# Performance work log

Measured on AMD Instinct MI355X. Metric: run time of the kernel, lower is better.

## Reference

```python
import jax, jax.numpy as jnp
import numpy as np

IN_C, OUT_C, K, STRIDE, PAD = 128, 256, 3, 1, 1

def setup_inputs() -> dict:
    key = jax.random.key(0)
    kx, kw = jax.random.split(key)
    x = jax.random.normal(kx, (32, IN_C, 56, 56), dtype=jnp.float32)
    # xavier_uniform_ on W: bound = sqrt(6 / (fan_in + fan_out)), fan = C*K*K
    fan_in = IN_C * K * K
    fan_out = OUT_C * K * K
    bound = float(np.sqrt(6.0 / (fan_in + fan_out)))
    W = jax.random.uniform(kw, (OUT_C, IN_C, K, K), dtype=jnp.float32, minval=-bound, maxval=bound)
    b = jnp.zeros((OUT_C,), dtype=jnp.float32)
    return {"x": x, "W": W, "b": b}

def reference(x, W, b):
    # Direct conv: NCHW input, OIHW weights -> NCHW output
    out = jax.lax.conv_general_dilated(
        x, W,
        window_strides=(STRIDE, STRIDE),
        padding=[(PAD, PAD), (PAD, PAD)],
        dimension_numbers=("NCHW", "OIHW", "NCHW"),
    )
    return out + b[None, :, None, None]
```

## Files before the change

### kernel.cpp

```cpp
#include <hip/hip_runtime.h>


typedef unsigned short u16;
typedef _Float16 f16x8 __attribute__((ext_vector_type(8)));
typedef float f32x4 __attribute__((ext_vector_type(4)));

#define CIN    128
#define COUT   256
#define HW     56
#define NPIX   3136
#define TOTPIX 100352
#define NKT    18

#define WAITVM0 asm volatile("s_waitcnt vmcnt(0)" ::: "memory")
#define BARRIER asm volatile("s_barrier" ::: "memory")

__device__ __forceinline__ void gload16(const void* g, void* l) {
  __builtin_amdgcn_global_load_lds(
      (const __attribute__((address_space(1))) void*)g,
      (__attribute__((address_space(3))) void*)l, 16, 0, 0);
}

__device__ __forceinline__ u16 f2h(float f) {
  _Float16 h = (_Float16)f;
  return __builtin_bit_cast(u16, h);
}

__global__ void prep_w(const float* __restrict__ W, u16* __restrict__ Wt,
                       u16* __restrict__ zp) {
  int e = blockIdx.x * 256 + threadIdx.x;
  if (blockIdx.x == 0 && threadIdx.x < 128) zp[threadIdx.x] = 0;
  int j   = e & 7;
  int ocl = (e >> 3) & 127;
  int k8  = (e >> 10) & 7;
  int o   = (e >> 13) & 1;
  int t   = e >> 14;
  int oc = o * 128 + ocl;
  int ic = (t & 1) * 64 + k8 * 8 + j;
  Wt[e] = f2h(W[(oc * CIN + ic) * 9 + (t >> 1)]);
}

__global__ void prep_x(const float* __restrict__ x, u16* __restrict__ xt) {
  __shared__ unsigned int tile[64 * 65];
  int b = blockIdx.x;
  int n = b / 49;
  int hw0 = (b % 49) * 64;
  int tid = threadIdx.x;
  const float* xb = x + (size_t)n * CIN * NPIX + hw0;
  #pragma unroll
  for (int i = 0; i < 16; ++i) {
    int e = tid + i * 256;
    int icp = e >> 6;
    int pix = e & 63;
    float a = xb[(size_t)(2 * icp) * NPIX + pix];
    float c = xb[(size_t)(2 * icp + 1) * NPIX + pix];
    tile[pix * 65 + icp] = (unsigned)f2h(a) | ((unsigned)f2h(c) << 16);
  }
  __syncthreads();
  #pragma unroll
  for (int i = 0; i < 4; ++i) {
    int e = tid + i * 256;
    int g = e >> 6;
    int pix = e & 63;
    uint4 v;
    v.x = tile[pix * 65 + g * 4 + 0];
    v.y = tile[pix * 65 + g * 4 + 1];
    v.z = tile[pix * 65 + g * 4 + 2];
    v.w = tile[pix * 65 + g * 4 + 3];
    *(uint4*)(xt + ((size_t)(n * 16 + g) * NPIX + hw0 + pix) * 8) = v;
  }
}

__global__ __launch_bounds__(512, 4) void conv_mfma(
    const u16* __restrict__ Wt, const u16* __restrict__ xt,
    const float* __restrict__ bias, float* __restrict__ out,
    const u16* __restrict__ zp) {
  __shared__ __align__(16) u16 lds[24576];

  int tid  = threadIdx.x;
  int lane = tid & 63;
  int wv   = tid >> 6;
  int bid  = blockIdx.x;
  int wgid = (bid & 7) * 98 + (bid >> 3);
  int octile = wgid & 1;
  int ptile  = wgid >> 1;

  int wm = wv >> 2, wn = wv & 3;
  int l15 = lane & 15, lg = lane >> 4;

  int spix = tid & 255;
  int sk8  = tid >> 8;
  int p = ptile * 256 + spix;
  int n = p / NPIX, r = p % NPIX, y = r / HW, xx = r % HW;
  const char* xtb = (const char*)xt;
  const char* wsrc = (const char*)Wt + (size_t)octile * 16384 + tid * 16;
  const char* zpc = (const char*)zp;

  auto stageA = [&](int t) {
    const char* src = wsrc + (size_t)t * 32768;
    gload16(src, &lds[tid * 8]);
    gload16(src + 8192, &lds[tid * 8 + 4096]);
  };
  auto stageB = [&](int t) {
    int tap = t >> 1, ich = t & 1;
    int t3 = tap / 3;
    int dh = t3 - 1, dw = (tap - t3 * 3) - 1;
    int iy = y + dh, ix = xx + dw;
    bool ok = (unsigned)iy < HW && (unsigned)ix < HW;
    const char* s0 = ok
        ? xtb + ((size_t)(n * 16 + ich * 8 + sk8) * NPIX + (r + dh * HW + dw)) * 16
        : zpc;
    size_t step = ok ? (size_t)2 * NPIX * 16 : 0;
    #pragma unroll
    for (int i = 0; i < 4; ++i)
      gload16(s0 + i * step, &lds[8192 + ((sk8 + 2 * i) * 256 + spix) * 8]);
  };

  f32x4 acc[4][4] = {};

  auto compute = [&]() {
    #pragma unroll
    for (int kk = 0; kk < 2; ++kk) {
      const u16* ab = &lds[((kk * 4 + lg) * 128 + wm * 64 + l15) * 8];
      const u16* bb = &lds[8192 + ((kk * 4 + lg) * 256 + wn * 64 + l15) * 8];
      f16x8 af[4], bf[4];
      #pragma unroll
      for (int q = 0; q < 4; ++q) af[q] = *(const f16x8*)&ab[q * 128];
      #pragma unroll
      for (int q = 0; q < 4; ++q) bf[q] = *(const f16x8*)&bb[q * 128];
      __builtin_amdgcn_s_setprio(1);
      #pragma unroll
      for (int mq = 0; mq < 4; ++mq)
        #pragma unroll
        for (int nf = 0; nf < 4; ++nf)
          acc[mq][nf] = __builtin_amdgcn_mfma_f32_16x16x32_f16(
              af[mq], bf[nf], acc[mq][nf], 0, 0, 0);
      __builtin_amdgcn_s_setprio(0);
    }
  };

  stageA(0); stageB(0);
  WAITVM0; BARRIER;
  for (int t = 0; t < NKT; ++t) {
    compute();
    if (t + 1 < NKT) {
      BARRIER;
      stageA(t + 1); stageB(t + 1);
      WAITVM0; BARRIER;
    }
  }

  float* ob[4];
  #pragma unroll
  for (int nf = 0; nf < 4; ++nf) {
    int pp = ptile * 256 + wn * 64 + nf * 16 + l15;
    int nn = pp / NPIX, hw = pp % NPIX;
    ob[nf] = out + (size_t)nn * COUT * NPIX + hw;
  }
  #pragma unroll
  for (int mq = 0; mq < 4; ++mq) {
    int oc = octile * 128 + wm * 64 + mq * 16 + lg * 4;
    f32x4 bv = *(const f32x4*)&bias[oc];
    #pragma unroll
    for (int rr = 0; rr < 4; ++rr) {
      size_t row = (size_t)(oc + rr) * NPIX;
      #pragma unroll
      for (int nf = 0; nf < 4; ++nf)
        ob[nf][row] = acc[mq][nf][rr] + bv[rr];
    }
  }
}

__global__ void conv_naive(const float* __restrict__ x, const float* __restrict__ W,
                           const float* __restrict__ b, float* __restrict__ out) {
  int idx = blockIdx.x * 256 + threadIdx.x;
  int hw = idx % NPIX;
  int tmp = idx / NPIX;
  int oc = tmp % COUT;
  int n = tmp / COUT;
  int h = hw / HW, w = hw % HW;
  float acc = b[oc];
  for (int ic = 0; ic < CIN; ++ic) {
    const float* xr = x + (size_t)(n * CIN + ic) * NPIX;
    const float* wr = W + (size_t)(oc * CIN + ic) * 9;
    #pragma unroll
    for (int kh = 0; kh < 3; ++kh) {
      int ih = h + kh - 1;
      if ((unsigned)ih >= HW) continue;
      #pragma unroll
      for (int kw = 0; kw < 3; ++kw) {
        int iw = w + kw - 1;
        if ((unsigned)iw >= HW) continue;
        acc += xr[ih * HW + iw] * wr[kh * 3 + kw];
      }
    }
  }
  out[idx] = acc;
}

extern "C" void kernel_launch(void* const* d_in, const int* in_sizes, int n_in,
                              void* d_out, int out_size, void* d_ws, size_t ws_size,
                              hipStream_t stream) {
  const float* x = (const float*)d_in[0];
  const float* W = (const float*)d_in[1];
  const float* b = (const float*)d_in[2];
  float* out = (float*)d_out;

  const size_t ZP_OFF = 0;
  const size_t WT_OFF = 256;
  const size_t XT_OFF = 256 + 589824;
  const size_t NEED = XT_OFF + (size_t)TOTPIX * CIN * 2;

  if (ws_size < NEED) {
    conv_naive<<<TOTPIX * COUT / 256, 256, 0, stream>>>(x, W, b, out);
    return;
  }
  char* ws = (char*)d_ws;
  u16* zp = (u16*)(ws + ZP_OFF);
  u16* Wt = (u16*)(ws + WT_OFF);
  u16* xt = (u16*)(ws + XT_OFF);

  prep_w<<<1152, 256, 0, stream>>>(W, Wt, zp);
  prep_x<<<1568, 256, 0, stream>>>(x, xt);
  conv_mfma<<<784, 512, 0, stream>>>(Wt, xt, b, out, zp);
}
```

Measured before the change: 91.91 us.

## Load activation fragments directly from global and double-buffer weight tiles in LDS

Activation (B) operands are no longer staged through LDS. Each lane loads its f16x8 fragments directly from global memory, using precomputed base offsets and a bitmask of which taps are in bounds, with padding taps reading a shared zero buffer. Weight tiles are now double-buffered in LDS, so the next tile's load is issued before the current compute and the barrier before staging is dropped. This shrinks LDS use and removes a barrier per step, but global loads now sit directly in front of the MFMAs and neighbouring waves re-read overlapping activation data through cache instead of from shared LDS.

Result: slower. 104.6 us (+13.8%).

```diff
diff --git a/kernel.cpp b/kernel.cpp
--- a/kernel.cpp
+++ b/kernel.cpp
@@ -75,7 +75,7 @@
     const u16* __restrict__ Wt, const u16* __restrict__ xt,
     const float* __restrict__ bias, float* __restrict__ out,
     const u16* __restrict__ zp) {
-  __shared__ __align__(16) u16 lds[24576];
+  __shared__ __align__(16) u16 lds[16384];
 
   int tid  = threadIdx.x;
   int lane = tid & 63;
@@ -88,46 +88,58 @@
   int wm = wv >> 2, wn = wv & 3;
   int l15 = lane & 15, lg = lane >> 4;
 
-  int spix = tid & 255;
-  int sk8  = tid >> 8;
-  int p = ptile * 256 + spix;
-  int n = p / NPIX, r = p % NPIX, y = r / HW, xx = r % HW;
-  const char* xtb = (const char*)xt;
+  const char* xtb  = (const char*)xt;
+  const char* zpc  = (const char*)zp;
   const char* wsrc = (const char*)Wt + (size_t)octile * 16384 + tid * 16;
-  const char* zpc = (const char*)zp;
+
+  unsigned boff[4];
+  unsigned long long vmask = 0ull;
+  #pragma unroll
+  for (int nf = 0; nf < 4; ++nf) {
+    int p = ptile * 256 + wn * 64 + nf * 16 + l15;
+    int n = p / NPIX, r = p % NPIX, y = r / HW, x = r % HW;
+    boff[nf] = (unsigned)(((n * 16 + lg) * NPIX + r) * 16);
+    #pragma unroll
+    for (int tap = 0; tap < 9; ++tap) {
+      int dh = tap / 3 - 1, dw = tap % 3 - 1;
+      unsigned long long ok =
+          ((unsigned)(y + dh) < HW && (unsigned)(x + dw) < HW) ? 1ull : 0ull;
+      vmask |= ok << (nf * 9 + tap);
+    }
+  }
 
   auto stageA = [&](int t) {
     const char* src = wsrc + (size_t)t * 32768;
-    gload16(src, &lds[tid * 8]);
-    gload16(src + 8192, &lds[tid * 8 + 4096]);
+    u16* dst = &lds[(t & 1) * 8192 + tid * 8];
+    gload16(src, dst);
+    gload16(src + 8192, dst + 4096);
   };
-  auto stageB = [&](int t) {
+
+  f32x4 acc[4][4] = {};
+
+  stageA(0);
+  WAITVM0; BARRIER;
+
+  for (int t = 0; t < NKT; ++t) {
     int tap = t >> 1, ich = t & 1;
-    int t3 = tap / 3;
-    int dh = t3 - 1, dw = (tap - t3 * 3) - 1;
-    int iy = y + dh, ix = xx + dw;
-    bool ok = (unsigned)iy < HW && (unsigned)ix < HW;
-    const char* s0 = ok
-        ? xtb + ((size_t)(n * 16 + ich * 8 + sk8) * NPIX + (r + dh * HW + dw)) * 16
-        : zpc;
-    size_t step = ok ? (size_t)2 * NPIX * 16 : 0;
-    #pragma unroll
-    for (int i = 0; i < 4; ++i)
-      gload16(s0 + i * step, &lds[8192 + ((sk8 + 2 * i) * 256 + spix) * 8]);
-  };
-
-  f32x4 acc[4][4] = {};
-
-  auto compute = [&]() {
+    int dh = tap / 3 - 1, dw = tap % 3 - 1;
+    int sh16 = ((dh * HW + dw) + ich * 8 * NPIX) * 16;
+    const u16* abase = &lds[(t & 1) * 8192];
+    if (t + 1 < NKT) stageA(t + 1);
     #pragma unroll
     for (int kk = 0; kk < 2; ++kk) {
-      const u16* ab = &lds[((kk * 4 + lg) * 128 + wm * 64 + l15) * 8];
-      const u16* bb = &lds[8192 + ((kk * 4 + lg) * 256 + wn * 64 + l15) * 8];
-      f16x8 af[4], bf[4];
-      #pragma unroll
-      for (int q = 0; q < 4; ++q) af[q] = *(const f16x8*)&ab[q * 128];
-      #pragma unroll
-      for (int q = 0; q < 4; ++q) bf[q] = *(const f16x8*)&bb[q * 128];
+      f16x8 bf[4], af[4];
+      #pragma unroll
+      for (int nf = 0; nf < 4; ++nf) {
+        bool ok = (vmask >> (nf * 9 + tap)) & 1ull;
+        const char* sp = ok ? xtb + ((int)boff[nf] + sh16 + kk * 4 * NPIX * 16)
+                            : zpc;
+        bf[nf] = *(const f16x8*)sp;
+      }
+      #pragma unroll
+      for (int q = 0; q < 4; ++q)
+        af[q] = *(const f16x8*)
+            &abase[((kk * 4 + lg) * 128 + wm * 64 + q * 16 + l15) * 8];
       __builtin_amdgcn_s_setprio(1);
       #pragma unroll
       for (int mq = 0; mq < 4; ++mq)
@@ -137,17 +149,8 @@
               af[mq], bf[nf], acc[mq][nf], 0, 0, 0);
       __builtin_amdgcn_s_setprio(0);
     }
-  };
-
-  stageA(0); stageB(0);
-  WAITVM0; BARRIER;
-  for (int t = 0; t < NKT; ++t) {
-    compute();
-    if (t + 1 < NKT) {
-      BARRIER;
-      stageA(t + 1); stageB(t + 1);
-      WAITVM0; BARRIER;
-    }
+    WAITVM0;
+    BARRIER;
   }
 
   float* ob[4];
```

## Double-buffer LDS stages and switch to 32x32x16 MFMA with halved K-steps

Applied to the files above, without the earlier changes.

Splits each K tile into two half-depth stages, which doubles the stage count. These stages are double-buffered in LDS so the global-to-LDS loads for the next stage are issued before computing on the current one. This removes one barrier per step and overlaps memory with MFMA. The 16x16x32 MFMAs are replaced with 32x32x16 MFMAs (2x2 per wave), which cuts LDS fragment reads per FLOP. The cost is more loop iterations and barriers, and a changed output register mapping in the epilogue.

Measured after the change: 101.3 us. +10.3%, slower.

```diff
diff --git a/kernel.cpp b/kernel.cpp
--- a/kernel.cpp
+++ b/kernel.cpp
@@ -4,13 +4,14 @@
 typedef unsigned short u16;
 typedef _Float16 f16x8 __attribute__((ext_vector_type(8)));
 typedef float f32x4 __attribute__((ext_vector_type(4)));
+typedef float f32x16 __attribute__((ext_vector_type(16)));
 
 #define CIN    128
 #define COUT   256
 #define HW     56
 #define NPIX   3136
 #define TOTPIX 100352
-#define NKT    18
+#define NKT    36
 
 #define WAITVM0 asm volatile("s_waitcnt vmcnt(0)" ::: "memory")
 #define BARRIER asm volatile("s_barrier" ::: "memory")
@@ -86,87 +87,87 @@
   int ptile  = wgid >> 1;
 
   int wm = wv >> 2, wn = wv & 3;
-  int l15 = lane & 15, lg = lane >> 4;
+  int l31 = lane & 31, lh = lane >> 5;
 
   int spix = tid & 255;
-  int sk8  = tid >> 8;
   int p = ptile * 256 + spix;
-  int n = p / NPIX, r = p % NPIX, y = r / HW, xx = r % HW;
-  const char* xtb = (const char*)xt;
-  const char* wsrc = (const char*)Wt + (size_t)octile * 16384 + tid * 16;
-  const char* zpc = (const char*)zp;
-
-  auto stageA = [&](int t) {
-    const char* src = wsrc + (size_t)t * 32768;
-    gload16(src, &lds[tid * 8]);
-    gload16(src + 8192, &lds[tid * 8 + 4096]);
-  };
-  auto stageB = [&](int t) {
-    int tap = t >> 1, ich = t & 1;
+  int sn = p / NPIX, sr = p % NPIX, sy = sr / HW, sx = sr % HW;
+  const char* xtb  = (const char*)xt;
+  const char* zpc  = (const char*)zp;
+  const char* wbase = (const char*)Wt + (size_t)octile * 16384 +
+                      ((tid >> 7) * 128 + (tid & 127)) * 16;
+
+  auto stage = [&](int s, int buf) {
+    const char* asrc = wbase + (size_t)(s >> 1) * 32768 + (s & 1) * 8192;
+    gload16(asrc, &lds[buf * 12288 + tid * 8]);
+    int tap = s >> 2, icq = s & 3;
     int t3 = tap / 3;
     int dh = t3 - 1, dw = (tap - t3 * 3) - 1;
-    int iy = y + dh, ix = xx + dw;
-    bool ok = (unsigned)iy < HW && (unsigned)ix < HW;
-    const char* s0 = ok
-        ? xtb + ((size_t)(n * 16 + ich * 8 + sk8) * NPIX + (r + dh * HW + dw)) * 16
+    bool ok = (unsigned)(sy + dh) < HW && (unsigned)(sx + dw) < HW;
+    const char* bsrc = ok
+        ? xtb + ((size_t)(sn * 16 + icq * 4 + (tid >> 8)) * NPIX +
+                 (sr + dh * HW + dw)) * 16
         : zpc;
     size_t step = ok ? (size_t)2 * NPIX * 16 : 0;
+    u16* bdst = &lds[buf * 12288 + 4096 + ((tid >> 8) * 256 + spix) * 8];
+    gload16(bsrc, bdst);
+    gload16(bsrc + step, bdst + 2 * 256 * 8);
+  };
+
+  f32x16 acc[2][2] = {};
+
+  stage(0, 0);
+  WAITVM0; BARRIER;
+
+  #pragma unroll 4
+  for (int s = 0; s < NKT; ++s) {
+    int buf = s & 1;
+    if (s + 1 < NKT) stage(s + 1, buf ^ 1);
+    const u16* base = &lds[buf * 12288];
     #pragma unroll
-    for (int i = 0; i < 4; ++i)
-      gload16(s0 + i * step, &lds[8192 + ((sk8 + 2 * i) * 256 + spix) * 8]);
-  };
-
-  f32x4 acc[4][4] = {};
-
-  auto compute = [&]() {
-    #pragma unroll
-    for (int kk = 0; kk < 2; ++kk) {
-      const u16* ab = &lds[((kk * 4 + lg) * 128 + wm * 64 + l15) * 8];
-      const u16* bb = &lds[8192 + ((kk * 4 + lg) * 256 + wn * 64 + l15) * 8];
-      f16x8 af[4], bf[4];
-      #pragma unroll
-      for (int q = 0; q < 4; ++q) af[q] = *(const f16x8*)&ab[q * 128];
-      #pragma unroll
-      for (int q = 0; q < 4; ++q) bf[q] = *(const f16x8*)&bb[q * 128];
+    for (int ks = 0; ks < 2; ++ks) {
+      int k8 = 2 * ks + lh;
+      f16x8 af[2], bf[2];
+      #pragma unroll
+      for (int mq = 0; mq < 2; ++mq)
+        af[mq] = *(const f16x8*)&base[(k8 * 128 + wm * 64 + mq * 32 + l31) * 8];
+      #pragma unroll
+      for (int nf = 0; nf < 2; ++nf)
+        bf[nf] = *(const f16x8*)
+            &base[4096 + (k8 * 256 + wn * 64 + nf * 32 + l31) * 8];
       __builtin_amdgcn_s_setprio(1);
       #pragma unroll
-      for (int mq = 0; mq < 4; ++mq)
+      for (int mq = 0; mq < 2; ++mq)
         #pragma unroll
-        for (int nf = 0; nf < 4; ++nf)
-          acc[mq][nf] = __builtin_amdgcn_mfma_f32_16x16x32_f16(
+        for (int nf = 0; nf < 2; ++nf)
+          acc[mq][nf] = __builtin_amdgcn_mfma_f32_32x32x16_f16(
               af[mq], bf[nf], acc[mq][nf], 0, 0, 0);
       __builtin_amdgcn_s_setprio(0);
     }
-  };
-
-  stageA(0); stageB(0);
-  WAITVM0; BARRIER;
-  for (int t = 0; t < NKT; ++t) {
-    compute();
-    if (t + 1 < NKT) {
-      BARRIER;
-      stageA(t + 1); stageB(t + 1);
-      WAITVM0; BARRIER;
-    }
-  }
-
-  float* ob[4];
-  #pragma unroll
-  for (int nf = 0; nf < 4; ++nf) {
-    int pp = ptile * 256 + wn * 64 + nf * 16 + l15;
+    WAITVM0;
+    BARRIER;
+  }
+
+  float* ob[2];
+  #pragma unroll
+  for (int nf = 0; nf < 2; ++nf) {
+    int pp = ptile * 256 + wn * 64 + nf * 32 + l31;
     int nn = pp / NPIX, hw = pp % NPIX;
     ob[nf] = out + (size_t)nn * COUT * NPIX + hw;
   }
   #pragma unroll
-  for (int mq = 0; mq < 4; ++mq) {
-    int oc = octile * 128 + wm * 64 + mq * 16 + lg * 4;
-    f32x4 bv = *(const f32x4*)&bias[oc];
+  for (int mq = 0; mq < 2; ++mq) {
     #pragma unroll
-    for (int rr = 0; rr < 4; ++rr) {
-      size_t row = (size_t)(oc + rr) * NPIX;
-      #pragma unroll
-      for (int nf = 0; nf < 4; ++nf)
-        ob[nf][row] = acc[mq][nf][rr] + bv[rr];
+    for (int rq = 0; rq < 4; ++rq) {
+      int ocg = octile * 128 + wm * 64 + mq * 32 + rq * 8 + lh * 4;
+      f32x4 bv = *(const f32x4*)&bias[ocg];
+      #pragma unroll
+      for (int j = 0; j < 4; ++j) {
+        size_t row = (size_t)(ocg + j) * NPIX;
+        #pragma unroll
+        for (int nf = 0; nf < 2; ++nf)
+          ob[nf][row] = acc[mq][nf][rq * 4 + j] + bv[j];
+      }
     }
   }
 }
```

## Halve conv pixel tile to 128 with 4-wave blocks and drop LDS transpose in prep_x

Applied to the files above, without the earlier changes.

The main conv kernel moves from 512-thread blocks with 256-pixel tiles to 256-thread blocks with 128-pixel tiles. This doubles the grid to 1568 blocks and cuts LDS per block, so more blocks can run per CU and the wave count is spread more evenly. In exchange, each pixel tile gets less reuse of the weight tile. prep_x is also rewritten to convert and pack 8 channels per pixel directly from global memory, with no LDS transpose.

After: 90.53 us, median of 2. No clear change (-1.5%).

```diff
diff --git a/kernel.cpp b/kernel.cpp
--- a/kernel.cpp
+++ b/kernel.cpp
@@ -41,93 +41,91 @@
 }
 
 __global__ void prep_x(const float* __restrict__ x, u16* __restrict__ xt) {
-  __shared__ unsigned int tile[64 * 65];
   int b = blockIdx.x;
-  int n = b / 49;
-  int hw0 = (b % 49) * 64;
-  int tid = threadIdx.x;
-  const float* xb = x + (size_t)n * CIN * NPIX + hw0;
-  #pragma unroll
-  for (int i = 0; i < 16; ++i) {
-    int e = tid + i * 256;
-    int icp = e >> 6;
-    int pix = e & 63;
-    float a = xb[(size_t)(2 * icp) * NPIX + pix];
-    float c = xb[(size_t)(2 * icp + 1) * NPIX + pix];
-    tile[pix * 65 + icp] = (unsigned)f2h(a) | ((unsigned)f2h(c) << 16);
-  }
-  __syncthreads();
+  int n = b >> 6, g = (b >> 2) & 15, c = b & 3;
+  const float* xs = x + ((size_t)(n * 16 + g) * 8) * NPIX;
+  u16* xd = xt + ((size_t)(n * 16 + g) * NPIX) * 8;
   #pragma unroll
   for (int i = 0; i < 4; ++i) {
-    int e = tid + i * 256;
-    int g = e >> 6;
-    int pix = e & 63;
-    uint4 v;
-    v.x = tile[pix * 65 + g * 4 + 0];
-    v.y = tile[pix * 65 + g * 4 + 1];
-    v.z = tile[pix * 65 + g * 4 + 2];
-    v.w = tile[pix * 65 + g * 4 + 3];
-    *(uint4*)(xt + ((size_t)(n * 16 + g) * NPIX + hw0 + pix) * 8) = v;
-  }
-}
-
-__global__ __launch_bounds__(512, 4) void conv_mfma(
+    int off = i * 256 + (int)threadIdx.x;
+    if (off < 784) {
+      int pix = c * 784 + off;
+      unsigned q0, q1, q2, q3;
+      q0 = (unsigned)f2h(xs[(size_t)0 * NPIX + pix]) |
+           ((unsigned)f2h(xs[(size_t)1 * NPIX + pix]) << 16);
+      q1 = (unsigned)f2h(xs[(size_t)2 * NPIX + pix]) |
+           ((unsigned)f2h(xs[(size_t)3 * NPIX + pix]) << 16);
+      q2 = (unsigned)f2h(xs[(size_t)4 * NPIX + pix]) |
+           ((unsigned)f2h(xs[(size_t)5 * NPIX + pix]) << 16);
+      q3 = (unsigned)f2h(xs[(size_t)6 * NPIX + pix]) |
+           ((unsigned)f2h(xs[(size_t)7 * NPIX + pix]) << 16);
+      uint4 v; v.x = q0; v.y = q1; v.z = q2; v.w = q3;
+      *(uint4*)(xd + (size_t)pix * 8) = v;
+    }
+  }
+}
+
+__global__ __launch_bounds__(256, 4) void conv_mfma(
     const u16* __restrict__ Wt, const u16* __restrict__ xt,
     const float* __restrict__ bias, float* __restrict__ out,
     const u16* __restrict__ zp) {
-  __shared__ __align__(16) u16 lds[24576];
+  __shared__ __align__(16) u16 lds[16384];
 
   int tid  = threadIdx.x;
   int lane = tid & 63;
   int wv   = tid >> 6;
   int bid  = blockIdx.x;
-  int wgid = (bid & 7) * 98 + (bid >> 3);
+  int wgid = (bid & 7) * 196 + (bid >> 3);
   int octile = wgid & 1;
   int ptile  = wgid >> 1;
 
-  int wm = wv >> 2, wn = wv & 3;
+  int wm = wv >> 1, wn = wv & 1;
   int l15 = lane & 15, lg = lane >> 4;
 
-  int spix = tid & 255;
-  int sk8  = tid >> 8;
-  int p = ptile * 256 + spix;
-  int n = p / NPIX, r = p % NPIX, y = r / HW, xx = r % HW;
+  int spix = tid & 127;
+  int p = ptile * 128 + spix;
+  int sn = p / NPIX, sr = p % NPIX, sy = sr / HW, sx = sr % HW;
   const char* xtb = (const char*)xt;
-  const char* wsrc = (const char*)Wt + (size_t)octile * 16384 + tid * 16;
   const char* zpc = (const char*)zp;
-
-  auto stageA = [&](int t) {
-    const char* src = wsrc + (size_t)t * 32768;
-    gload16(src, &lds[tid * 8]);
-    gload16(src + 8192, &lds[tid * 8 + 4096]);
-  };
-  auto stageB = [&](int t) {
+  const char* wbase = (const char*)Wt + (size_t)octile * 16384 + tid * 16;
+
+  auto stage = [&](int t) {
+    const char* asrc = wbase + (size_t)t * 32768;
+    #pragma unroll
+    for (int i = 0; i < 4; ++i)
+      gload16(asrc + i * 4096, &lds[tid * 8 + i * 2048]);
     int tap = t >> 1, ich = t & 1;
     int t3 = tap / 3;
     int dh = t3 - 1, dw = (tap - t3 * 3) - 1;
-    int iy = y + dh, ix = xx + dw;
-    bool ok = (unsigned)iy < HW && (unsigned)ix < HW;
-    const char* s0 = ok
-        ? xtb + ((size_t)(n * 16 + ich * 8 + sk8) * NPIX + (r + dh * HW + dw)) * 16
+    bool ok = (unsigned)(sy + dh) < HW && (unsigned)(sx + dw) < HW;
+    const char* bsrc = ok
+        ? xtb + ((size_t)(sn * 16 + ich * 8 + (tid >> 7)) * NPIX +
+                 (sr + dh * HW + dw)) * 16
         : zpc;
     size_t step = ok ? (size_t)2 * NPIX * 16 : 0;
+    u16* bdst = &lds[8192 + ((tid >> 7) * 128 + spix) * 8];
     #pragma unroll
     for (int i = 0; i < 4; ++i)
-      gload16(s0 + i * step, &lds[8192 + ((sk8 + 2 * i) * 256 + spix) * 8]);
+      gload16(bsrc + i * step, bdst + i * 2048);
   };
 
   f32x4 acc[4][4] = {};
 
-  auto compute = [&]() {
+  stage(0);
+  WAITVM0; BARRIER;
+
+  for (int t = 0; t < NKT; ++t) {
     #pragma unroll
     for (int kk = 0; kk < 2; ++kk) {
-      const u16* ab = &lds[((kk * 4 + lg) * 128 + wm * 64 + l15) * 8];
-      const u16* bb = &lds[8192 + ((kk * 4 + lg) * 256 + wn * 64 + l15) * 8];
       f16x8 af[4], bf[4];
       #pragma unroll
-      for (int q = 0; q < 4; ++q) af[q] = *(const f16x8*)&ab[q * 128];
-      #pragma unroll
-      for (int q = 0; q < 4; ++q) bf[q] = *(const f16x8*)&bb[q * 128];
+      for (int q = 0; q < 4; ++q)
+        af[q] = *(const f16x8*)
+            &lds[((kk * 4 + lg) * 128 + wm * 64 + q * 16 + l15) * 8];
+      #pragma unroll
+      for (int q = 0; q < 4; ++q)
+        bf[q] = *(const f16x8*)
+            &lds[8192 + ((kk * 4 + lg) * 128 + wn * 64 + q * 16 + l15) * 8];
       __builtin_amdgcn_s_setprio(1);
       #pragma unroll
       for (int mq = 0; mq < 4; ++mq)
@@ -137,15 +135,9 @@
               af[mq], bf[nf], acc[mq][nf], 0, 0, 0);
       __builtin_amdgcn_s_setprio(0);
     }
-  };
-
-  stageA(0); stageB(0);
-  WAITVM0; BARRIER;
-  for (int t = 0; t < NKT; ++t) {
-    compute();
     if (t + 1 < NKT) {
       BARRIER;
-      stageA(t + 1); stageB(t + 1);
+      stage(t + 1);
       WAITVM0; BARRIER;
     }
   }
@@ -153,7 +145,7 @@
   float* ob[4];
   #pragma unroll
   for (int nf = 0; nf < 4; ++nf) {
-    int pp = ptile * 256 + wn * 64 + nf * 16 + l15;
+    int pp = ptile * 128 + wn * 64 + nf * 16 + l15;
     int nn = pp / NPIX, hw = pp % NPIX;
     ob[nf] = out + (size_t)nn * COUT * NPIX + hw;
   }
@@ -221,6 +213,6 @@
   u16* xt = (u16*)(ws + XT_OFF);
 
   prep_w<<<1152, 256, 0, stream>>>(W, Wt, zp);
-  prep_x<<<1568, 256, 0, stream>>>(x, xt);
-  conv_mfma<<<784, 512, 0, stream>>>(Wt, xt, b, out, zp);
-}
+  prep_x<<<2048, 256, 0, stream>>>(x, xt);
+  conv_mfma<<<1568, 256, 0, stream>>>(Wt, xt, b, out, zp);
+}
```
